# Kernel optimization log

Hardware: AMD Instinct MI355X
Metric: run time of the kernel (lower is better)

Reference implementation:

```python
import jax, jax.numpy as jnp
import numpy as np

DIM = 2048
N_HEADS = 16
Q_RANK = 1536
KV_RANK = 512
D_NOPE = 128
D_ROPE = 64
D_V = 128
EPS = 1e-6
B, S = 2, 2048
ROPE_THETA = 10000.0


def rmsnorm(x, w, eps=EPS):
    return x * jax.lax.rsqrt(jnp.mean(x * x, axis=-1, keepdims=True) + eps) * w


def apply_rope(x):
    # x: [b, h, s, d] with d even; LLaMA-style interleaved pair rotation
    b, h, s, d = x.shape
    inv_freq = 1.0 / (ROPE_THETA ** (jnp.arange(0, d, 2, dtype=jnp.float32) / d))
    ang = jnp.arange(s, dtype=jnp.float32)[:, None] * inv_freq[None, :]  # [s, d/2]
    cos, sin = jnp.cos(ang), jnp.sin(ang)
    xr = x.reshape(b, h, s, d // 2, 2)
    x1, x2 = xr[..., 0], xr[..., 1]
    o1 = x1 * cos - x2 * sin
    o2 = x1 * sin + x2 * cos
    return jnp.stack([o1, o2], axis=-1).reshape(b, h, s, d)


def setup_inputs() -> dict:
    key = jax.random.key(0)
    ks = jax.random.split(key, 10)
    std = 0.02
    return {
        "x": jax.random.normal(ks[0], (B, S, DIM), dtype=jnp.float32),
        "wq_down": jax.random.normal(ks[1], (Q_RANK, DIM), dtype=jnp.float32) * std,
        "q_norm_w": jnp.ones((Q_RANK,), dtype=jnp.float32),
        "wq_up": jax.random.normal(ks[2], (N_HEADS * D_NOPE, Q_RANK), dtype=jnp.float32) * std,
        "wq_rope": jax.random.normal(ks[3], (N_HEADS * D_ROPE, Q_RANK), dtype=jnp.float32) * std,
        "wkv_down": jax.random.normal(ks[4], (KV_RANK, DIM), dtype=jnp.float32) * std,
        "kv_norm_w": jnp.ones((KV_RANK,), dtype=jnp.float32),
        "wkv_up": jax.random.normal(ks[5], (N_HEADS * (D_NOPE + D_V), KV_RANK), dtype=jnp.float32) * std,
        "wk_rope": jax.random.normal(ks[6], (D_ROPE, DIM), dtype=jnp.float32) * std,
        "wo": jax.random.normal(ks[7], (DIM, N_HEADS * D_V), dtype=jnp.float32) * std,
    }


def reference(x, wq_down, q_norm_w, wq_up, wq_rope, wkv_down, kv_norm_w, wkv_up, wk_rope, wo):
    bs, s, _ = x.shape
    # low-rank Q path
    q_c = rmsnorm(x @ wq_down.T, q_norm_w)                              # [b,s,qr]
    q_nope = (q_c @ wq_up.T).reshape(bs, s, N_HEADS, D_NOPE).transpose(0, 2, 1, 3)
    q_pe = (q_c @ wq_rope.T).reshape(bs, s, N_HEADS, D_ROPE).transpose(0, 2, 1, 3)
    # low-rank KV path
    kv_c = rmsnorm(x @ wkv_down.T, kv_norm_w)                           # [b,s,kvr]
    kv_up = (kv_c @ wkv_up.T).reshape(bs, s, N_HEADS, D_NOPE + D_V)
    k_nope = kv_up[..., :D_NOPE].transpose(0, 2, 1, 3)                  # [b,h,s,dn]
    v = kv_up[..., D_NOPE:].transpose(0, 2, 1, 3)                       # [b,h,s,dv]
    # shared rope key (1 head), broadcast across heads
    k_rope = (x @ wk_rope.T).reshape(bs, s, 1, D_ROPE).transpose(0, 2, 1, 3)  # [b,1,s,dr]
    q_pe = apply_rope(q_pe)
    k_rope = apply_rope(k_rope)
    q = jnp.concatenate([q_nope, q_pe], axis=-1)                        # [b,h,s,dn+dr]
    k = jnp.concatenate([k_nope, jnp.broadcast_to(k_rope, (bs, N_HEADS, s, D_ROPE))], axis=-1)
    scale = 1.0 / np.sqrt(D_NOPE + D_ROPE)
    scores = jnp.einsum('bhqd,bhkd->bhqk', q, k) * scale                # [b,h,s,s]
    causal = jnp.tril(jnp.ones((s, s), dtype=bool))
    scores = jnp.where(causal, scores, -jnp.inf)
    probs = jax.nn.softmax(scores, axis=-1)
    out = jnp.einsum('bhqk,bhkv->bhqv', probs, v)                       # [b,h,s,dv]
    out = out.transpose(0, 2, 1, 3).reshape(bs, s, N_HEADS * D_V)
    return out @ wo.T
```

## Files before the change

### kernel.cpp

```cpp
#include <hip/hip_runtime.h>
#include <stdint.h>

typedef _Float16 f16x8 __attribute__((ext_vector_type(8)));
typedef _Float16 f16x4 __attribute__((ext_vector_type(4)));
typedef float fx4 __attribute__((ext_vector_type(4)));

static constexpr int S_LEN = 2048;
static constexpr int BATCH = 2;
static constexpr int TOKENS = BATCH * S_LEN;
static constexpr int DIM = 2048;
static constexpr int NH = 16;
static constexpr int QR = 1536;
static constexpr int KVR = 512;
static constexpr int DN = 128;
static constexpr int DR = 64;
static constexpr int DV = 128;

__device__ __forceinline__ void async16(const _Float16* g, _Float16* lds_base_uniform) {
  __builtin_amdgcn_global_load_lds(
      (const __attribute__((address_space(1))) void*)g,
      (__attribute__((address_space(3))) void*)lds_base_uniform, 16, 0, 0);
}

__device__ __forceinline__ void bar() {
  asm volatile("" ::: "memory");
  __builtin_amdgcn_s_barrier();
  asm volatile("" ::: "memory");
}
#define VMWAIT(n) asm volatile("s_waitcnt vmcnt(" #n ")" ::: "memory")

#define ROR16(x, ctrl) \
  __uint_as_float(__builtin_amdgcn_update_dpp(__float_as_uint(x), __float_as_uint(x), \
                                              (ctrl), 0xF, 0xF, false))

struct CvtSegs {
  const float* src[8];
  _Float16* dst[8];
  int n4[8];
  int cum[9];
};
__global__ __launch_bounds__(256) void cvt_all(CvtSegs s) {
  const int b = blockIdx.x;
  int seg = 0;
#pragma unroll
  for (int k = 0; k < 7; ++k) seg += (b >= s.cum[seg + 1]) ? 1 : 0;
  const int i = (b - s.cum[seg]) * 256 + threadIdx.x;
  if (i >= s.n4[seg]) return;
  fx4 v = *(const fx4*)(s.src[seg] + (size_t)i * 4);
  f16x4 o;
  o[0] = (_Float16)v[0]; o[1] = (_Float16)v[1];
  o[2] = (_Float16)v[2]; o[3] = (_Float16)v[3];
  *(f16x4*)(s.dst[seg] + (size_t)i * 4) = o;
}

template <int MODE>
__global__ __launch_bounds__(256) void gemm_nt(const _Float16* __restrict__ A,
                                               const _Float16* __restrict__ W,
                                               void* __restrict__ C0v,
                                               void* __restrict__ C1v,
                                               int M, int N, int K) {
  __shared__ __attribute__((aligned(16))) _Float16 As[3][128 * 32];
  __shared__ __attribute__((aligned(16))) _Float16 Ws[3][128 * 32];
  const int tid = threadIdx.x;
  const int lane = tid & 63;
  const int wave = tid >> 6;
  const int wr = (wave >> 1) * 64;
  const int wc = (wave & 1) * 64;
  const int m16 = lane & 15;
  const int quad = lane >> 4;
  const int m0 = blockIdx.y * 128;
  const int n0 = blockIdx.x * 128;

  auto stage = [&](int buf, int k0) {
#pragma unroll
    for (int p = 0; p < 2; ++p) {
      const int cb = p * 256 + wave * 64;
      const int ch = cb + lane;
      const int r = ch >> 2;
      const int c8 = (ch & 3) * 8;
      async16(A + (size_t)(m0 + r) * K + k0 + c8, &As[buf][cb * 8]);
      async16(W + (size_t)(n0 + r) * K + k0 + c8, &Ws[buf][cb * 8]);
    }
  };

  const fx4 fz = {0.f, 0.f, 0.f, 0.f};
  fx4 acc[4][4];
#pragma unroll
  for (int i = 0; i < 4; ++i)
#pragma unroll
    for (int j = 0; j < 4; ++j) acc[i][j] = fz;

  const int nkt = K >> 5;
  stage(0, 0);
  stage(1, 32);
  int cur = 0;
  for (int kt = 0; kt < nkt; ++kt) {
    if (kt + 1 < nkt) { VMWAIT(4); } else { VMWAIT(0); }
    bar();
    if (kt + 2 < nkt) {
      int b2 = cur + 2; if (b2 >= 3) b2 -= 3;
      stage(b2, (kt + 2) * 32);
    }
    const _Float16* as = As[cur];
    const _Float16* ws = Ws[cur];
    f16x8 af[4], wf[4];
#pragma unroll
    for (int i = 0; i < 4; ++i)
      af[i] = *(const f16x8*)(&as[(wr + i * 16 + m16) * 32 + quad * 8]);
#pragma unroll
    for (int j = 0; j < 4; ++j)
      wf[j] = *(const f16x8*)(&ws[(wc + j * 16 + m16) * 32 + quad * 8]);
#pragma unroll
    for (int i = 0; i < 4; ++i)
#pragma unroll
      for (int j = 0; j < 4; ++j)
        acc[i][j] = __builtin_amdgcn_mfma_f32_16x16x32_f16(af[i], wf[j], acc[i][j], 0, 0, 0);
    if (++cur == 3) cur = 0;
  }

#pragma unroll
  for (int j = 0; j < 4; ++j) {
    const int col = n0 + wc + j * 16 + m16;
    if (MODE == 2) {
      _Float16* KN = (_Float16*)C0v;
      _Float16* VT = (_Float16*)C1v;
      const int head = col >> 8;
      const int sub = col & 255;
      if (sub < 128) {
#pragma unroll
        for (int i = 0; i < 4; ++i)
#pragma unroll
          for (int r = 0; r < 4; ++r)
            KN[(size_t)(m0 + wr + i * 16 + quad * 4 + r) * 2048 + head * 128 + sub] =
                (_Float16)acc[i][j][r];
      } else {
        const int dv = sub - 128;
#pragma unroll
        for (int i = 0; i < 4; ++i) {
          f16x4 v;
#pragma unroll
          for (int r = 0; r < 4; ++r) v[r] = (_Float16)acc[i][j][r];
          *(f16x4*)(&VT[(size_t)(head * 128 + dv) * TOKENS + m0 + wr + i * 16 + quad * 4]) = v;
        }
      }
    } else if (MODE == 3) {
#pragma unroll
      for (int i = 0; i < 4; ++i)
#pragma unroll
        for (int r = 0; r < 4; ++r) {
          const size_t row = (size_t)(m0 + wr + i * 16 + quad * 4 + r);
          if (col < 2048) ((_Float16*)C0v)[row * 2048 + col] = (_Float16)acc[i][j][r];
          else ((_Float16*)C1v)[row * 1024 + col - 2048] = (_Float16)acc[i][j][r];
        }
    } else if (MODE == 4) {
      if (col < 576) {
#pragma unroll
        for (int i = 0; i < 4; ++i)
#pragma unroll
          for (int r = 0; r < 4; ++r) {
            const size_t row = (size_t)(m0 + wr + i * 16 + quad * 4 + r);
            if (col < 512) ((_Float16*)C0v)[row * 512 + col] = (_Float16)acc[i][j][r];
            else ((_Float16*)C1v)[row * 64 + col - 512] = (_Float16)acc[i][j][r];
          }
      }
    } else {
      if (col < N) {
#pragma unroll
        for (int i = 0; i < 4; ++i)
#pragma unroll
          for (int r = 0; r < 4; ++r) {
            const size_t row = (size_t)(m0 + wr + i * 16 + quad * 4 + r);
            if (MODE == 0) ((_Float16*)C0v)[row * N + col] = (_Float16)acc[i][j][r];
            else ((float*)C0v)[row * N + col] = acc[i][j][r];
          }
      }
    }
  }
}

template <int NC>
__global__ __launch_bounds__(256) void rmsnorm_ip(_Float16* __restrict__ xx,
                                                  const float* __restrict__ w) {
  const int row = blockIdx.x;
  _Float16* p = xx + (size_t)row * NC;
  float ss = 0.f;
  for (int c = threadIdx.x; c < NC; c += 256) {
    const float v = (float)p[c];
    ss += v * v;
  }
#pragma unroll
  for (int d = 1; d < 64; d <<= 1) ss += __shfl_xor(ss, d);
  __shared__ float red[4];
  if ((threadIdx.x & 63) == 0) red[threadIdx.x >> 6] = ss;
  __syncthreads();
  const float rs = rsqrtf((red[0] + red[1] + red[2] + red[3]) * (1.0f / NC) + 1e-6f);
  for (int c = threadIdx.x; c < NC; c += 256)
    p[c] = (_Float16)((float)p[c] * rs * w[c]);
}

__global__ void rope_q(_Float16* __restrict__ qpe) {
  const int idx = blockIdx.x * 256 + threadIdx.x;
  const int t = idx >> 9;
  const int rem = idx & 511;
  const int hh = rem >> 5;
  const int i = rem & 31;
  const int s = t & (S_LEN - 1);
  const float fr = exp2f(-(float)i * 0.4152410118609203f);
  const float ang = (float)s * fr;
  const float sn = sinf(ang), cs = cosf(ang);
  const size_t base = (size_t)t * (NH * DR) + hh * DR + 2 * i;
  const float x1 = (float)qpe[base];
  const float x2 = (float)qpe[base + 1];
  qpe[base] = (_Float16)(x1 * cs - x2 * sn);
  qpe[base + 1] = (_Float16)(x1 * sn + x2 * cs);
}

__global__ void rope_k(_Float16* __restrict__ kr) {
  const int idx = blockIdx.x * 256 + threadIdx.x;
  const int t = idx >> 5;
  const int i = idx & 31;
  const int s = t & (S_LEN - 1);
  const float fr = exp2f(-(float)i * 0.4152410118609203f);
  const float ang = (float)s * fr;
  const float sn = sinf(ang), cs = cosf(ang);
  const size_t base = (size_t)t * DR + 2 * i;
  const float x1 = (float)kr[base];
  const float x2 = (float)kr[base + 1];
  kr[base] = (_Float16)(x1 * cs - x2 * sn);
  kr[base + 1] = (_Float16)(x1 * sn + x2 * cs);
}

__global__ __launch_bounds__(256, 2) void mla_attn(
    const _Float16* __restrict__ qn,
    const _Float16* __restrict__ qp,
    const _Float16* __restrict__ kn,
    const _Float16* __restrict__ kr,
    const _Float16* __restrict__ vT,
    _Float16* __restrict__ out)
{
  __shared__ __attribute__((aligned(16))) _Float16 Ks[3][768 * 8];
  __shared__ __attribute__((aligned(16))) _Float16 Vs[3][512 * 8];
  __shared__ __attribute__((aligned(16))) _Float16 Ps[4][16][40];

  const int bid = blockIdx.x;
  const int b = bid >> 8;
  const int u = bid & 255;
  const int h = u >> 4;
  const int jp = u & 15;
  const int tok0 = b * S_LEN;

  const int tid = threadIdx.x;
  const int lane = tid & 63;
  const int wave = tid >> 6;
  const int m16 = lane & 15;
  const int quad = lane >> 4;

  auto stageKV = [&](int buf, int kbase) {
#pragma unroll
    for (int j = 0; j < 3; ++j) {
      const int i = wave * 3 + j;
      const int ch = i * 2 + (lane >> 5);
      const int key = lane & 31;
      const _Float16* g = (ch < 16)
          ? kn + (size_t)(tok0 + kbase + key) * 2048 + h * 128 + ch * 8
          : kr + (size_t)(tok0 + kbase + key) * 64 + (ch - 16) * 8;
      async16(g, &Ks[buf][i * 512]);
    }
#pragma unroll
    for (int j = 0; j < 2; ++j) {
      const int i = wave * 2 + j;
      const int p = i * 64 + lane;
      const int L = p ^ ((p >> 3) & 3);
      const int dv = L >> 2;
      const int qc = L & 3;
      async16(vT + (size_t)(h * 128 + dv) * TOKENS + tok0 + kbase + qc * 8,
              &Vs[buf][i * 512]);
    }
  };

  const float scale2 = 0.07216878364870323f * 1.4426950408889634f;
  const fx4 fz = {0.f, 0.f, 0.f, 0.f};

  for (int half = 0; half < 2; ++half) {
    const int q32 = half ? (31 - jp) : jp;
    const int qb = q32 * 64;
    const int R0 = qb + wave * 16;

    f16x8 qf[6];
    {
      const size_t t = (size_t)(tok0 + qb + wave * 16 + m16);
#pragma unroll
      for (int kk = 0; kk < 4; ++kk)
        qf[kk] = *(const f16x8*)(qn + t * 2048 + h * 128 + kk * 32 + quad * 8);
#pragma unroll
      for (int kk = 0; kk < 2; ++kk)
        qf[4 + kk] = *(const f16x8*)(qp + t * 1024 + h * 64 + kk * 32 + quad * 8);
    }

    fx4 oacc[8];
#pragma unroll
    for (int n = 0; n < 8; ++n) oacc[n] = fz;
    float mst[4], lst[4];
#pragma unroll
    for (int r = 0; r < 4; ++r) { mst[r] = -3.0e38f; lst[r] = 0.f; }

    const int nkt = (qb >> 5) + 2;

    bar();
    stageKV(0, 0);
    stageKV(1, 32);
    int cur = 0;
    for (int kt = 0; kt < nkt; ++kt) {
      const int kbase = kt * 32;
      if (kt + 1 < nkt) { VMWAIT(5); } else { VMWAIT(0); }
      bar();
      if (kt + 2 < nkt) {
        int b2 = cur + 2; if (b2 >= 3) b2 -= 3;
        stageKV(b2, kbase + 64);
      }
      const bool live = (kbase <= R0 + 15);
      if (!live) { if (++cur == 3) cur = 0; continue; }
      const _Float16* ks = Ks[cur];
      const _Float16* vs = Vs[cur];

      fx4 sc[2];
      sc[0] = fz; sc[1] = fz;
      __builtin_amdgcn_s_setprio(1);
#pragma unroll
      for (int kk = 0; kk < 6; ++kk) {
#pragma unroll
        for (int n = 0; n < 2; ++n) {
          f16x8 kf = *(const f16x8*)(&ks[(kk * 128 + quad * 32 + n * 16 + m16) * 8]);
          sc[n] = __builtin_amdgcn_mfma_f32_16x16x32_f16(qf[kk], kf, sc[n], 0, 0, 0);
        }
      }
      __builtin_amdgcn_s_setprio(0);

      f16x8 vf[8];
#pragma unroll
      for (int n8 = 0; n8 < 8; ++n8) {
        const int c0 = (n8 * 16 + m16) * 4 + quad;
        vf[n8] = *(const f16x8*)(&vs[(c0 ^ ((c0 >> 3) & 3)) * 8]);
      }

      const bool needmask = (kbase + 31 > R0);
      float alpha[4];
      bool any_upd = false;
#pragma unroll
      for (int r = 0; r < 4; ++r) {
        float v0 = sc[0][r] * scale2;
        float v1 = sc[1][r] * scale2;
        if (needmask) {
          const int qrow = R0 + quad * 4 + r;
          if (kbase + m16 > qrow)      v0 = -3.0e38f;
          if (kbase + 16 + m16 > qrow) v1 = -3.0e38f;
        }
        float mx = fmaxf(v0, v1);
        mx = fmaxf(mx, ROR16(mx, 0x128));
        mx = fmaxf(mx, ROR16(mx, 0x124));
        mx = fmaxf(mx, ROR16(mx, 0x122));
        mx = fmaxf(mx, ROR16(mx, 0x121));
        float al = 1.0f;
        if (__any(mx > mst[r] + 10.0f)) {
          const float mn = fmaxf(mst[r], mx);
          al = exp2f(mst[r] - mn);
          mst[r] = mn;
          any_upd = true;
        }
        alpha[r] = al;
        const float p0 = exp2f(v0 - mst[r]);
        const float p1 = exp2f(v1 - mst[r]);
        float ls = p0 + p1;
        ls += ROR16(ls, 0x128);
        ls += ROR16(ls, 0x124);
        ls += ROR16(ls, 0x122);
        ls += ROR16(ls, 0x121);
        lst[r] = lst[r] * al + ls;
        _Float16* pr = &Ps[wave][quad * 4 + r][0];
        pr[m16] = (_Float16)p0;
        pr[16 + m16] = (_Float16)p1;
      }
      if (any_upd) {
#pragma unroll
        for (int n8 = 0; n8 < 8; ++n8)
#pragma unroll
          for (int r = 0; r < 4; ++r) oacc[n8][r] *= alpha[r];
      }

      f16x8 pf = *(const f16x8*)(&Ps[wave][m16][quad * 8]);
      __builtin_amdgcn_s_setprio(1);
#pragma unroll
      for (int n8 = 0; n8 < 8; ++n8)
        oacc[n8] = __builtin_amdgcn_mfma_f32_16x16x32_f16(pf, vf[n8], oacc[n8], 0, 0, 0);
      __builtin_amdgcn_s_setprio(0);
      if (++cur == 3) cur = 0;
    }

    float inv[4];
#pragma unroll
    for (int r = 0; r < 4; ++r) inv[r] = 1.0f / lst[r];
#pragma unroll
    for (int n8 = 0; n8 < 8; ++n8) {
#pragma unroll
      for (int r = 0; r < 4; ++r) {
        const size_t t = (size_t)(tok0 + qb + wave * 16 + quad * 4 + r);
        out[t * 2048 + h * 128 + n8 * 16 + m16] = (_Float16)(oacc[n8][r] * inv[r]);
      }
    }
  }
}

extern "C" void kernel_launch(void* const* d_in, const int* in_sizes, int n_in,
                              void* d_out, int out_size, void* d_ws, size_t ws_size,
                              hipStream_t stream) {
  const float* x         = (const float*)d_in[0];
  const float* wq_down   = (const float*)d_in[1];
  const float* q_norm_w  = (const float*)d_in[2];
  const float* wq_up     = (const float*)d_in[3];
  const float* wq_rope   = (const float*)d_in[4];
  const float* wkv_down  = (const float*)d_in[5];
  const float* kv_norm_w = (const float*)d_in[6];
  const float* wkv_up    = (const float*)d_in[7];
  const float* wk_rope   = (const float*)d_in[8];
  const float* wo        = (const float*)d_in[9];
  float* out = (float*)d_out;

  char* ws = (char*)d_ws;
  size_t off = 0;
  auto alloc = [&](size_t bytes) {
    char* p = ws + off;
    off += (bytes + 255) & ~(size_t)255;
    return p;
  };
  _Float16* x_h     = (_Float16*)alloc((size_t)TOKENS * DIM * 2);
  _Float16* wqd_h   = (_Float16*)alloc((size_t)QR * DIM * 2);
  _Float16* wquqr_h = (_Float16*)alloc((size_t)3072 * QR * 2);
  _Float16* wkvdr_h = (_Float16*)alloc((size_t)576 * DIM * 2);
  _Float16* wkvu_h  = (_Float16*)alloc((size_t)NH * 256 * KVR * 2);
  _Float16* wo_h    = (_Float16*)alloc((size_t)DIM * NH * DV * 2);
  _Float16* qc_h    = (_Float16*)alloc((size_t)TOKENS * QR * 2);
  _Float16* kvc_h   = (_Float16*)alloc((size_t)TOKENS * KVR * 2);
  _Float16* qnope_h = (_Float16*)alloc((size_t)TOKENS * 2048 * 2);
  _Float16* qpe_h   = (_Float16*)alloc((size_t)TOKENS * 1024 * 2);
  _Float16* knope_h = (_Float16*)alloc((size_t)TOKENS * 2048 * 2);
  _Float16* vT_h    = (_Float16*)alloc((size_t)2048 * TOKENS * 2);
  _Float16* krope_h = (_Float16*)alloc((size_t)TOKENS * DR * 2);
  _Float16* attn_h  = (_Float16*)alloc((size_t)TOKENS * 2048 * 2);

  CvtSegs cs;
  const float* srcs[8] = {x, wq_down, wq_up, wq_rope, wkv_down, wk_rope, wkv_up, wo};
  _Float16* dsts[8] = {x_h, wqd_h, wquqr_h, wquqr_h + (size_t)2048 * QR,
                       wkvdr_h, wkvdr_h + (size_t)512 * DIM, wkvu_h, wo_h};
  const size_t ns[8] = {(size_t)TOKENS * DIM, (size_t)QR * DIM, (size_t)2048 * QR,
                        (size_t)1024 * QR, (size_t)KVR * DIM, (size_t)DR * DIM,
                        (size_t)NH * 256 * KVR, (size_t)DIM * NH * DV};
  int cum = 0;
  for (int i = 0; i < 8; ++i) {
    cs.src[i] = srcs[i];
    cs.dst[i] = dsts[i];
    cs.n4[i] = (int)(ns[i] / 4);
    cs.cum[i] = cum;
    cum += (cs.n4[i] + 255) / 256;
  }
  cs.cum[8] = cum;
  cvt_all<<<dim3(cum), 256, 0, stream>>>(cs);

  auto gx = [](int n) { return (unsigned)((n + 127) / 128); };
  const unsigned gm = TOKENS / 128;

  gemm_nt<0><<<dim3(gx(QR), gm), 256, 0, stream>>>(x_h, wqd_h, qc_h, nullptr, TOKENS, QR, DIM);
  rmsnorm_ip<QR><<<dim3(TOKENS), 256, 0, stream>>>(qc_h, q_norm_w);
  gemm_nt<4><<<dim3(gx(576), gm), 256, 0, stream>>>(x_h, wkvdr_h, kvc_h, krope_h, TOKENS, 576, DIM);
  rmsnorm_ip<KVR><<<dim3(TOKENS), 256, 0, stream>>>(kvc_h, kv_norm_w);
  rope_k<<<dim3(TOKENS * 32 / 256), 256, 0, stream>>>(krope_h);
  gemm_nt<3><<<dim3(gx(3072), gm), 256, 0, stream>>>(qc_h, wquqr_h, qnope_h, qpe_h, TOKENS, 3072, QR);
  rope_q<<<dim3(TOKENS * NH * 32 / 256), 256, 0, stream>>>(qpe_h);
  gemm_nt<2><<<dim3(gx(4096), gm), 256, 0, stream>>>(kvc_h, wkvu_h, knope_h, vT_h, TOKENS, 4096, KVR);
  mla_attn<<<dim3(512), 256, 0, stream>>>(qnope_h, qpe_h, knope_h, krope_h, vT_h, attn_h);
  gemm_nt<1><<<dim3(gx(DIM), gm), 256, 0, stream>>>(attn_h, wo_h, out, nullptr, TOKENS, DIM, NH * DV);
}
```

Measured before the change: 532.5 us.

## Split attention into one block per query tile, heaviest-first, with double buffering

Replaces the paired-query-tile scheme (each block handled two complementary causal tiles) with 1024 blocks, each processing one 64-row query tile, scheduled longest-first. The KV staging drops from a triple-buffered async pipeline with vmcnt waits to a double buffer guarded by a plain __syncthreads. This aims to improve load balance and occupancy through smaller LDS use and more blocks. In exchange it gives up the explicit async-wait overlap and may leave prefetches less hidden.

```diff
diff --git a/kernel.cpp b/kernel.cpp
--- a/kernel.cpp
+++ b/kernel.cpp
@@ -238,15 +238,17 @@
     const _Float16* __restrict__ vT,
     _Float16* __restrict__ out)
 {
-  __shared__ __attribute__((aligned(16))) _Float16 Ks[3][768 * 8];
-  __shared__ __attribute__((aligned(16))) _Float16 Vs[3][512 * 8];
+  __shared__ __attribute__((aligned(16))) _Float16 Ks[2][768 * 8];
+  __shared__ __attribute__((aligned(16))) _Float16 Vs[2][512 * 8];
   __shared__ __attribute__((aligned(16))) _Float16 Ps[4][16][40];
 
   const int bid = blockIdx.x;
-  const int b = bid >> 8;
-  const int u = bid & 255;
-  const int h = u >> 4;
-  const int jp = u & 15;
+  const int j = bid >> 5;
+  const int bh = bid & 31;
+  const int b = bh >> 4;
+  const int h = bh & 15;
+  const int q32 = 31 - j;
+  const int qb = q32 * 64;
   const int tok0 = b * S_LEN;
 
   const int tid = threadIdx.x;
@@ -254,11 +256,12 @@
   const int wave = tid >> 6;
   const int m16 = lane & 15;
   const int quad = lane >> 4;
+  const int R0 = qb + wave * 16;
 
   auto stageKV = [&](int buf, int kbase) {
 #pragma unroll
-    for (int j = 0; j < 3; ++j) {
-      const int i = wave * 3 + j;
+    for (int jj = 0; jj < 3; ++jj) {
+      const int i = wave * 3 + jj;
       const int ch = i * 2 + (lane >> 5);
       const int key = lane & 31;
       const _Float16* g = (ch < 16)
@@ -267,8 +270,8 @@
       async16(g, &Ks[buf][i * 512]);
     }
 #pragma unroll
-    for (int j = 0; j < 2; ++j) {
-      const int i = wave * 2 + j;
+    for (int jj = 0; jj < 2; ++jj) {
+      const int i = wave * 2 + jj;
       const int p = i * 64 + lane;
       const int L = p ^ ((p >> 3) & 3);
       const int dv = L >> 2;
@@ -281,131 +284,118 @@
   const float scale2 = 0.07216878364870323f * 1.4426950408889634f;
   const fx4 fz = {0.f, 0.f, 0.f, 0.f};
 
-  for (int half = 0; half < 2; ++half) {
-    const int q32 = half ? (31 - jp) : jp;
-    const int qb = q32 * 64;
-    const int R0 = qb + wave * 16;
-
-    f16x8 qf[6];
-    {
-      const size_t t = (size_t)(tok0 + qb + wave * 16 + m16);
-#pragma unroll
-      for (int kk = 0; kk < 4; ++kk)
-        qf[kk] = *(const f16x8*)(qn + t * 2048 + h * 128 + kk * 32 + quad * 8);
-#pragma unroll
-      for (int kk = 0; kk < 2; ++kk)
-        qf[4 + kk] = *(const f16x8*)(qp + t * 1024 + h * 64 + kk * 32 + quad * 8);
-    }
-
-    fx4 oacc[8];
-#pragma unroll
-    for (int n = 0; n < 8; ++n) oacc[n] = fz;
-    float mst[4], lst[4];
-#pragma unroll
-    for (int r = 0; r < 4; ++r) { mst[r] = -3.0e38f; lst[r] = 0.f; }
-
-    const int nkt = (qb >> 5) + 2;
-
-    bar();
-    stageKV(0, 0);
-    stageKV(1, 32);
-    int cur = 0;
-    for (int kt = 0; kt < nkt; ++kt) {
-      const int kbase = kt * 32;
-      if (kt + 1 < nkt) { VMWAIT(5); } else { VMWAIT(0); }
-      bar();
-      if (kt + 2 < nkt) {
-        int b2 = cur + 2; if (b2 >= 3) b2 -= 3;
-        stageKV(b2, kbase + 64);
-      }
-      const bool live = (kbase <= R0 + 15);
-      if (!live) { if (++cur == 3) cur = 0; continue; }
-      const _Float16* ks = Ks[cur];
-      const _Float16* vs = Vs[cur];
-
-      fx4 sc[2];
-      sc[0] = fz; sc[1] = fz;
-      __builtin_amdgcn_s_setprio(1);
-#pragma unroll
-      for (int kk = 0; kk < 6; ++kk) {
-#pragma unroll
-        for (int n = 0; n < 2; ++n) {
-          f16x8 kf = *(const f16x8*)(&ks[(kk * 128 + quad * 32 + n * 16 + m16) * 8]);
-          sc[n] = __builtin_amdgcn_mfma_f32_16x16x32_f16(qf[kk], kf, sc[n], 0, 0, 0);
-        }
-      }
-      __builtin_amdgcn_s_setprio(0);
-
-      f16x8 vf[8];
-#pragma unroll
-      for (int n8 = 0; n8 < 8; ++n8) {
-        const int c0 = (n8 * 16 + m16) * 4 + quad;
-        vf[n8] = *(const f16x8*)(&vs[(c0 ^ ((c0 >> 3) & 3)) * 8]);
-      }
-
-      const bool needmask = (kbase + 31 > R0);
-      float alpha[4];
-      bool any_upd = false;
-#pragma unroll
-      for (int r = 0; r < 4; ++r) {
-        float v0 = sc[0][r] * scale2;
-        float v1 = sc[1][r] * scale2;
-        if (needmask) {
-          const int qrow = R0 + quad * 4 + r;
-          if (kbase + m16 > qrow)      v0 = -3.0e38f;
-          if (kbase + 16 + m16 > qrow) v1 = -3.0e38f;
-        }
-        float mx = fmaxf(v0, v1);
-        mx = fmaxf(mx, ROR16(mx, 0x128));
-        mx = fmaxf(mx, ROR16(mx, 0x124));
-        mx = fmaxf(mx, ROR16(mx, 0x122));
-        mx = fmaxf(mx, ROR16(mx, 0x121));
-        float al = 1.0f;
-        if (__any(mx > mst[r] + 10.0f)) {
-          const float mn = fmaxf(mst[r], mx);
-          al = exp2f(mst[r] - mn);
-          mst[r] = mn;
-          any_upd = true;
-        }
-        alpha[r] = al;
-        const float p0 = exp2f(v0 - mst[r]);
-        const float p1 = exp2f(v1 - mst[r]);
-        float ls = p0 + p1;
-        ls += ROR16(ls, 0x128);
-        ls += ROR16(ls, 0x124);
-        ls += ROR16(ls, 0x122);
-        ls += ROR16(ls, 0x121);
-        lst[r] = lst[r] * al + ls;
-        _Float16* pr = &Ps[wave][quad * 4 + r][0];
-        pr[m16] = (_Float16)p0;
-        pr[16 + m16] = (_Float16)p1;
-      }
-      if (any_upd) {
-#pragma unroll
-        for (int n8 = 0; n8 < 8; ++n8)
-#pragma unroll
-          for (int r = 0; r < 4; ++r) oacc[n8][r] *= alpha[r];
-      }
-
-      f16x8 pf = *(const f16x8*)(&Ps[wave][m16][quad * 8]);
-      __builtin_amdgcn_s_setprio(1);
+  f16x8 qf[6];
+  {
+    const size_t t = (size_t)(tok0 + qb + wave * 16 + m16);
+#pragma unroll
+    for (int kk = 0; kk < 4; ++kk)
+      qf[kk] = *(const f16x8*)(qn + t * 2048 + h * 128 + kk * 32 + quad * 8);
+#pragma unroll
+    for (int kk = 0; kk < 2; ++kk)
+      qf[4 + kk] = *(const f16x8*)(qp + t * 1024 + h * 64 + kk * 32 + quad * 8);
+  }
+
+  fx4 oacc[8];
+#pragma unroll
+  for (int n = 0; n < 8; ++n) oacc[n] = fz;
+  float mst[4], lst[4];
+#pragma unroll
+  for (int r = 0; r < 4; ++r) { mst[r] = -3.0e38f; lst[r] = 0.f; }
+
+  const int nkt = (qb >> 5) + 2;
+
+  stageKV(0, 0);
+  for (int kt = 0; kt < nkt; ++kt) {
+    const int kbase = kt * 32;
+    __syncthreads();
+    if (kt + 1 < nkt) stageKV((kt + 1) & 1, kbase + 32);
+
+    const bool live = (kbase <= R0 + 15);
+    if (!live) continue;
+    const _Float16* ks = Ks[kt & 1];
+    const _Float16* vs = Vs[kt & 1];
+
+    fx4 sc[2];
+    sc[0] = fz; sc[1] = fz;
+    __builtin_amdgcn_s_setprio(1);
+#pragma unroll
+    for (int kk = 0; kk < 6; ++kk) {
+#pragma unroll
+      for (int n = 0; n < 2; ++n) {
+        f16x8 kf = *(const f16x8*)(&ks[(kk * 128 + quad * 32 + n * 16 + m16) * 8]);
+        sc[n] = __builtin_amdgcn_mfma_f32_16x16x32_f16(qf[kk], kf, sc[n], 0, 0, 0);
+      }
+    }
+    __builtin_amdgcn_s_setprio(0);
+
+    f16x8 vf[8];
+#pragma unroll
+    for (int n8 = 0; n8 < 8; ++n8) {
+      const int c0 = (n8 * 16 + m16) * 4 + quad;
+      vf[n8] = *(const f16x8*)(&vs[(c0 ^ ((c0 >> 3) & 3)) * 8]);
+    }
+
+    const bool needmask = (kbase + 31 > R0);
+    float alpha[4];
+    bool any_upd = false;
+#pragma unroll
+    for (int r = 0; r < 4; ++r) {
+      float v0 = sc[0][r] * scale2;
+      float v1 = sc[1][r] * scale2;
+      if (needmask) {
+        const int qrow = R0 + quad * 4 + r;
+        if (kbase + m16 > qrow)      v0 = -3.0e38f;
+        if (kbase + 16 + m16 > qrow) v1 = -3.0e38f;
+      }
+      float mx = fmaxf(v0, v1);
+      mx = fmaxf(mx, ROR16(mx, 0x128));
+      mx = fmaxf(mx, ROR16(mx, 0x124));
+      mx = fmaxf(mx, ROR16(mx, 0x122));
+      mx = fmaxf(mx, ROR16(mx, 0x121));
+      float al = 1.0f;
+      if (__any(mx > mst[r] + 10.0f)) {
+        const float mn = fmaxf(mst[r], mx);
+        al = exp2f(mst[r] - mn);
+        mst[r] = mn;
+        any_upd = true;
+      }
+      alpha[r] = al;
+      const float p0 = exp2f(v0 - mst[r]);
+      const float p1 = exp2f(v1 - mst[r]);
+      float ls = p0 + p1;
+      ls += ROR16(ls, 0x128);
+      ls += ROR16(ls, 0x124);
+      ls += ROR16(ls, 0x122);
+      ls += ROR16(ls, 0x121);
+      lst[r] = lst[r] * al + ls;
+      _Float16* pr = &Ps[wave][quad * 4 + r][0];
+      pr[m16] = (_Float16)p0;
+      pr[16 + m16] = (_Float16)p1;
+    }
+    if (any_upd) {
 #pragma unroll
       for (int n8 = 0; n8 < 8; ++n8)
-        oacc[n8] = __builtin_amdgcn_mfma_f32_16x16x32_f16(pf, vf[n8], oacc[n8], 0, 0, 0);
-      __builtin_amdgcn_s_setprio(0);
-      if (++cur == 3) cur = 0;
-    }
-
-    float inv[4];
-#pragma unroll
-    for (int r = 0; r < 4; ++r) inv[r] = 1.0f / lst[r];
-#pragma unroll
-    for (int n8 = 0; n8 < 8; ++n8) {
-#pragma unroll
-      for (int r = 0; r < 4; ++r) {
-        const size_t t = (size_t)(tok0 + qb + wave * 16 + quad * 4 + r);
-        out[t * 2048 + h * 128 + n8 * 16 + m16] = (_Float16)(oacc[n8][r] * inv[r]);
-      }
+#pragma unroll
+        for (int r = 0; r < 4; ++r) oacc[n8][r] *= alpha[r];
+    }
+
+    f16x8 pf = *(const f16x8*)(&Ps[wave][m16][quad * 8]);
+    __builtin_amdgcn_s_setprio(1);
+#pragma unroll
+    for (int n8 = 0; n8 < 8; ++n8)
+      oacc[n8] = __builtin_amdgcn_mfma_f32_16x16x32_f16(pf, vf[n8], oacc[n8], 0, 0, 0);
+    __builtin_amdgcn_s_setprio(0);
+  }
+
+  float inv[4];
+#pragma unroll
+  for (int r = 0; r < 4; ++r) inv[r] = 1.0f / lst[r];
+#pragma unroll
+  for (int n8 = 0; n8 < 8; ++n8) {
+#pragma unroll
+    for (int r = 0; r < 4; ++r) {
+      const size_t t = (size_t)(tok0 + qb + wave * 16 + quad * 4 + r);
+      out[t * 2048 + h * 128 + n8 * 16 + m16] = (_Float16)(oacc[n8][r] * inv[r]);
     }
   }
 }
@@ -476,6 +466,6 @@
   gemm_nt<3><<<dim3(gx(3072), gm), 256, 0, stream>>>(qc_h, wquqr_h, qnope_h, qpe_h, TOKENS, 3072, QR);
   rope_q<<<dim3(TOKENS * NH * 32 / 256), 256, 0, stream>>>(qpe_h);
   gemm_nt<2><<<dim3(gx(4096), gm), 256, 0, stream>>>(kvc_h, wkvu_h, knope_h, vT_h, TOKENS, 4096, KVR);
-  mla_attn<<<dim3(512), 256, 0, stream>>>(qnope_h, qpe_h, knope_h, krope_h, vT_h, attn_h);
+  mla_attn<<<dim3(1024), 256, 0, stream>>>(qnope_h, qpe_h, knope_h, krope_h, vT_h, attn_h);
   gemm_nt<1><<<dim3(gx(DIM), gm), 256, 0, stream>>>(attn_h, wo_h, out, nullptr, TOKENS, DIM, NH * DV);
 }
```

Result: faster. 512.4 us (-3.8%).
